# Kernel optimization log

Hardware: AMD Instinct MI355X
Metric: run time of the kernel (lower is better)

The kernel has to match this reference:

```python
import jax, jax.numpy as jnp
import numpy as np


def _fft_conv(x, filts):
    # x: [B, inC, S, S] real; filts: [inC, outC, k, k, 2] (real/imag channels)
    # Matches FFT_Conv_Layer: zero-pad bottom/right by k-1, FFT, complex
    # multiply-accumulate over inC, inverse FFT, crop [1:-1, 1:-1], take real.
    N = x.shape[-1] + filts.shape[-2] - 1  # imgSize + filtSize - 1
    Fx = jnp.fft.fft2(x, s=(N, N))                      # [B, inC, N, N] complex
    fc = filts[..., 0] + 1j * filts[..., 1]             # [inC, outC, k, k] complex
    Ff = jnp.fft.fft2(fc, s=(N, N))                     # [inC, outC, N, N]
    prod = jnp.einsum('bihw,iohw->bohw', Fx, Ff)        # sum over inC, no huge 5D temp
    return jnp.real(jnp.fft.ifft2(prod))[:, :, 1:-1, 1:-1]


def _spectral_pool(x, fsize):
    # Keep lowest `fsize` frequencies (corner crop of the FFT), inverse FFT, ReLU.
    F = jnp.fft.fft2(x)
    n = (fsize - 1) // 2
    tl = F[:, :, :n + 1, :n + 1]
    tr = F[:, :, :n + 1, -n:]
    bl = F[:, :, -n:, :n + 1]
    br = F[:, :, -n:, -n:]
    top = jnp.concatenate([tl, tr], axis=-1)
    bot = jnp.concatenate([bl, br], axis=-1)
    out = jnp.real(jnp.fft.ifft2(jnp.concatenate([top, bot], axis=-2)))
    return jax.nn.relu(out)


def setup_inputs() -> dict:
    key = jax.random.key(0)
    ks = jax.random.split(key, 10)
    B = 16
    filt_shapes = [(3, 32), (32, 64), (64, 128), (128, 256), (256, 256)]
    inp = {'x': jax.random.normal(ks[0], (B, 3, 224, 224), dtype=jnp.float32)}
    for i, (ci, co) in enumerate(filt_shapes):
        inp[f'f{i + 1}'] = 0.01 * jax.random.normal(ks[1 + i], (ci, co, 3, 3, 2), dtype=jnp.float32)
    inp['gamma'] = jnp.ones((256,), jnp.float32)
    inp['beta'] = jnp.zeros((256,), jnp.float32)
    inp['W1'] = 0.02 * jax.random.normal(ks[6], (9216, 512), dtype=jnp.float32)
    inp['b1'] = jnp.zeros((512,), jnp.float32)
    inp['W2'] = 0.02 * jax.random.normal(ks[7], (512, 256), dtype=jnp.float32)
    inp['b2'] = jnp.zeros((256,), jnp.float32)
    inp['W3'] = 0.02 * jax.random.normal(ks[8], (256, 10), dtype=jnp.float32)
    inp['b3'] = jnp.zeros((10,), jnp.float32)
    return inp


def reference(x, f1, f2, f3, f4, f5, gamma, beta, W1, b1, W2, b2, W3, b3):
    h = _spectral_pool(_fft_conv(x, f1), 113)   # [B, 32, 113, 113]
    h = _spectral_pool(_fft_conv(h, f2), 55)    # [B, 64, 55, 55]
    h = _spectral_pool(_fft_conv(h, f3), 27)    # [B, 128, 27, 27]
    h = _spectral_pool(_fft_conv(h, f4), 13)    # [B, 256, 13, 13]
    h = _fft_conv(h, f5)                        # [B, 256, 13, 13]
    # BatchNorm2d (training mode: batch statistics, biased variance)
    mean = jnp.mean(h, axis=(0, 2, 3), keepdims=True)
    var = jnp.var(h, axis=(0, 2, 3), keepdims=True)
    h = (h - mean) * jax.lax.rsqrt(var + 1e-5)
    h = h * gamma.reshape(1, -1, 1, 1) + beta.reshape(1, -1, 1, 1)
    # AdaptiveAvgPool2d((6,6)) on 13x13 == avg pool, kernel 3, stride 2
    h = jax.lax.reduce_window(h, 0.0, jax.lax.add, (1, 1, 3, 3), (1, 1, 2, 2), 'VALID') / 9.0
    h = h.reshape(h.shape[0], -1)               # [B, 9216]
    # dropout omitted (deterministic reference)
    h = jax.nn.relu(h @ W1 + b1)
    h = jax.nn.relu(h @ W2 + b2)
    return jax.nn.log_softmax(h @ W3 + b3, axis=1)
```

## Files before the change

kernel.cpp:

```cpp
#include <hip/hip_runtime.h>
#include <hip/hip_bf16.h>

typedef __attribute__((ext_vector_type(8))) short short8_t;
typedef __attribute__((ext_vector_type(4))) float float4_t;

#define OFF_CF  0u
#define OFF_PB1 25690112u
#define OFF_PB2 38765568u
#define OFF_PB3 44960768u
#define OFF_PB4 47946752u
#define OFF_C5  49331200u
#define OFF_AP  52100096u
#define OFF_H1  52689920u
#define OFF_H2  52722688u
#define OFF_P   52739072u
#define OFF_FPK 53918720u
#define OFF_PPK 55874560u

static __device__ __forceinline__ unsigned short f2bf(float v) {
    __hip_bfloat16 h = __float2bfloat16(v);
    return *(unsigned short*)&h;
}
static __device__ __forceinline__ float bf2f(unsigned short u) {
    __hip_bfloat16 h = *(__hip_bfloat16*)&u;
    return __bfloat162float(h);
}
static __device__ __forceinline__ unsigned short ld_bf(const float* p) { return f2bf(*p); }
static __device__ __forceinline__ unsigned short ld_bf(const unsigned short* p) { return *p; }
static __device__ __forceinline__ void st_out(float* p, float v) { *p = v; }
static __device__ __forceinline__ void st_out(unsigned short* p, float v) { *p = f2bf(v); }

__global__ void pack_f_k(const float* __restrict__ f, unsigned short* __restrict__ A,
                         int Ci, int Co) {
    int id = blockIdx.x * 256 + threadIdx.x;
    int nci = Ci >> 5;
    int total = (Co >> 4) * nci * 9 * 512;
    if (id >= total) return;
    int j = id & 7, lane = (id >> 3) & 63;
    int uv = (id >> 9) % 9;
    int rest = id / (512 * 9);
    int cc = rest % nci, co_blk = rest / nci;
    int m = lane & 15, k = ((lane >> 4) << 3) + j;
    int ci = (cc << 5) + k, co = (co_blk << 4) + m;
    A[id] = f2bf(f[((size_t)(ci * Co + co) * 9 + uv) * 2]);
}

__global__ void pack_f1_k(const float* __restrict__ f, unsigned short* __restrict__ A) {
    int id = blockIdx.x * 256 + threadIdx.x;
    if (id >= 2 * 512) return;
    int j = id & 7, lane = (id >> 3) & 63, co_blk = id >> 9;
    int m = lane & 15, k = ((lane >> 4) << 3) + j;
    float v = 0.f;
    if (k < 27) {
        int ci = k / 9, uv = k % 9;
        v = f[((size_t)(ci * 32 + co_blk * 16 + m) * 9 + uv) * 2];
    }
    A[id] = f2bf(v);
}

__global__ void pack_pool_k(unsigned short* __restrict__ P, int M, int N, int RT, int KC) {
    int id = blockIdx.x * 256 + threadIdx.x;
    if (id >= RT * KC * 512) return;
    int j = id & 7, lane = (id >> 3) & 63;
    int c = (id >> 9) % KC, rt = id / (512 * KC);
    int row = (rt << 4) + (lane & 15);
    int col = (c << 5) + ((lane >> 4) << 3) + j;
    double val = 0.0;
    if (row < M && col < N) {
        int n = (M - 1) / 2;
        double w = 6.283185307179586476925286766559 *
                   ((double)row / (double)M - (double)col / (double)N);
        double acc = 1.0;
        for (int a = 1; a <= n; ++a) acc += 2.0 * cos(w * (double)a);
        val = acc / (double)M;
    }
    float vf = (float)val;
    unsigned short hi = f2bf(vf);
    unsigned short lo = f2bf(vf - bf2f(hi));
    size_t base = ((size_t)(rt * KC + c) * 2) * 512 + lane * 8 + j;
    P[base] = hi;
    P[base + 512] = lo;
}

#define CPAD 40
template<typename Tin, typename Tout>
__global__ void conv_mfma_k(const Tin* __restrict__ x, const unsigned short* __restrict__ Apk,
                            Tout* __restrict__ y, int Ci, int Co, int H) {
    __shared__ unsigned short xs[3 * 34 * CPAD];
    int p = blockIdx.z % H, b = blockIdx.z / H;
    int q0 = blockIdx.x << 5;
    int co0 = blockIdx.y << 5;
    int tid = threadIdx.x;
    int lane = tid & 63, w = tid >> 6;
    int co_sub = w >> 1, n_sub = w & 1;
    int n_off = n_sub << 4;
    int nci = Ci >> 5;
    int kb = ((lane >> 4) << 3);
    float4_t acc = {0.f, 0.f, 0.f, 0.f};
    const Tin* xb = x + (size_t)b * Ci * H * H;
    int co_blk = (co0 >> 4) + co_sub;
    for (int cc = 0; cc < nci; ++cc) {
        for (int e = tid; e < 32 * 3 * 34; e += 256) {
            int ci = e / 102, rc = e % 102, r = rc / 34, c = rc % 34;
            int gp = p - 1 + r, gq = q0 - 1 + c;
            unsigned short v = 0;
            if ((unsigned)gp < (unsigned)H && (unsigned)gq < (unsigned)H)
                v = ld_bf(&xb[((size_t)((cc << 5) + ci) * H + gp) * H + gq]);
            xs[(r * 34 + c) * CPAD + ci] = v;
        }
        __syncthreads();
        const unsigned short* Ap = Apk + (((size_t)co_blk * nci + cc) * 9) * 512;
#pragma unroll
        for (int uv = 0; uv < 9; ++uv) {
            int u = uv / 3, v = uv % 3;
            short8_t af = *(const short8_t*)(Ap + ((uv * 64 + lane) << 3));
            int r = 2 - u;
            int c = n_off + (lane & 15) + 2 - v;
            short8_t bf = *(const short8_t*)(&xs[(r * 34 + c) * CPAD + kb]);
            acc = __builtin_amdgcn_mfma_f32_16x16x32_bf16(af, bf, acc, 0, 0, 0);
        }
        __syncthreads();
    }
    int n = lane & 15, mg = (lane >> 4) << 2;
    int q = q0 + n_off + n;
    if (q < H) {
        Tout* yb = y + (((size_t)b * Co + co0 + (co_sub << 4)) * H + p) * H + q;
#pragma unroll
        for (int r2 = 0; r2 < 4; ++r2)
            st_out(&yb[(size_t)(mg + r2) * H * H], acc[r2]);
    }
}

template<typename Tout>
__global__ void conv1_mfma_k(const float* __restrict__ x, const unsigned short* __restrict__ Apk,
                             Tout* __restrict__ y, int H) {
    __shared__ unsigned short xs[32 * CPAD];
    int p = blockIdx.z % H, b = blockIdx.z / H;
    int q0 = blockIdx.x << 5;
    int tid = threadIdx.x;
    int lane = tid & 63, w = tid >> 6;
    int co_sub = w >> 1, n_sub = w & 1;
    int n_off = n_sub << 4;
    int kb = ((lane >> 4) << 3);
    const float* xb = x + (size_t)b * 3 * H * H;
    for (int e = tid; e < 1024; e += 256) {
        int n = e >> 5, k = e & 31;
        float val = 0.f;
        if (k < 27) {
            int ci = k / 9, uv = k % 9, u = uv / 3, v = uv % 3;
            int gp = p + 1 - u, gq = q0 + n + 1 - v;
            if ((unsigned)gp < (unsigned)H && (unsigned)gq < (unsigned)H)
                val = xb[((size_t)ci * H + gp) * H + gq];
        }
        xs[n * CPAD + k] = f2bf(val);
    }
    __syncthreads();
    short8_t af = *(const short8_t*)(Apk + ((co_sub * 64 + lane) << 3));
    short8_t bf = *(const short8_t*)(&xs[(n_off + (lane & 15)) * CPAD + kb]);
    float4_t acc = {0.f, 0.f, 0.f, 0.f};
    acc = __builtin_amdgcn_mfma_f32_16x16x32_bf16(af, bf, acc, 0, 0, 0);
    int n = lane & 15, mg = (lane >> 4) << 2;
    int q = q0 + n_off + n;
    if (q < H) {
        Tout* yb = y + (((size_t)b * 32 + (co_sub << 4)) * H + p) * H + q;
#pragma unroll
        for (int r2 = 0; r2 < 4; ++r2)
            st_out(&yb[(size_t)(mg + r2) * H * H], acc[r2]);
    }
}

template<int N, int M, int TRT>
__global__ __launch_bounds__(256) void pool_mfma_k(const float* __restrict__ x,
                                                   const unsigned short* __restrict__ PK,
                                                   unsigned short* __restrict__ out) {
    constexpr int MT = (N + 15) / 16;
    constexpr int RT = (M + 15) / 16;
    constexpr int KC = (N + 31) / 32;
    constexpr int XPAD = 40;
    constexpr int ZPAD = KC * 32 + 8;
    constexpr int XROWS = MT * 16;
    constexpr int NT1 = MT * TRT;
    constexpr int L1 = (NT1 + 3) / 4;
    constexpr int NT2 = RT * TRT;
    constexpr int L2 = (NT2 + 3) / 4;
    __shared__ unsigned short xh[XROWS * XPAD], xl[XROWS * XPAD];
    __shared__ unsigned short zh[16 * TRT * ZPAD], zl[16 * TRT * ZPAD];

    int t0g = blockIdx.x * TRT;
    int bc = blockIdx.y;
    int tid = threadIdx.x;
    int lane = tid & 63, w = tid >> 6;
    int l15 = lane & 15;
    int kb = (lane >> 4) << 3;
    const float* xb = x + (size_t)bc * N * N;

    float4_t acc[L1];
#pragma unroll
    for (int i = 0; i < L1; ++i) acc[i] = (float4_t){0.f, 0.f, 0.f, 0.f};

    for (int c = 0; c < KC; ++c) {
        for (int id = tid; id < XROWS * 32; id += 256) {
            int u = id >> 5, vv = id & 31, v = (c << 5) + vv;
            float val = (u < N && v < N) ? xb[u * N + v] : 0.f;
            unsigned short hi = f2bf(val);
            xh[u * XPAD + vv] = hi;
            xl[u * XPAD + vv] = f2bf(val - bf2f(hi));
        }
        __syncthreads();
#pragma unroll
        for (int li = 0; li < L1; ++li) {
            int idx = li * 4 + w;
            if (idx < NT1) {
                int mt = idx / TRT, nt = idx % TRT;
                short8_t ahi = *(const short8_t*)(&xh[(mt * 16 + l15) * XPAD + kb]);
                short8_t alo = *(const short8_t*)(&xl[(mt * 16 + l15) * XPAD + kb]);
                const unsigned short* bp =
                    PK + ((size_t)((t0g + nt) * KC + c) * 2) * 512 + lane * 8;
                short8_t bhi = *(const short8_t*)bp;
                short8_t blo = *(const short8_t*)(bp + 512);
                acc[li] = __builtin_amdgcn_mfma_f32_16x16x32_bf16(ahi, bhi, acc[li], 0, 0, 0);
                acc[li] = __builtin_amdgcn_mfma_f32_16x16x32_bf16(ahi, blo, acc[li], 0, 0, 0);
                acc[li] = __builtin_amdgcn_mfma_f32_16x16x32_bf16(alo, bhi, acc[li], 0, 0, 0);
            }
        }
        __syncthreads();
    }
#pragma unroll
    for (int li = 0; li < L1; ++li) {
        int idx = li * 4 + w;
        if (idx < NT1) {
            int mt = idx / TRT, nt = idx % TRT;
            int t = nt * 16 + l15;
            int u0 = mt * 16 + ((lane >> 4) << 2);
            unsigned short h0 = f2bf(acc[li][0]), h1 = f2bf(acc[li][1]);
            unsigned short h2 = f2bf(acc[li][2]), h3 = f2bf(acc[li][3]);
            unsigned long long ph =
                (unsigned long long)h0 | ((unsigned long long)h1 << 16) |
                ((unsigned long long)h2 << 32) | ((unsigned long long)h3 << 48);
            unsigned long long pl =
                (unsigned long long)f2bf(acc[li][0] - bf2f(h0)) |
                ((unsigned long long)f2bf(acc[li][1] - bf2f(h1)) << 16) |
                ((unsigned long long)f2bf(acc[li][2] - bf2f(h2)) << 32) |
                ((unsigned long long)f2bf(acc[li][3] - bf2f(h3)) << 48);
            *(unsigned long long*)(&zh[t * ZPAD + u0]) = ph;
            *(unsigned long long*)(&zl[t * ZPAD + u0]) = pl;
        }
    }
    __syncthreads();

    float4_t acc2[L2];
#pragma unroll
    for (int i = 0; i < L2; ++i) acc2[i] = (float4_t){0.f, 0.f, 0.f, 0.f};
    for (int c = 0; c < KC; ++c) {
#pragma unroll
        for (int li = 0; li < L2; ++li) {
            int idx = li * 4 + w;
            if (idx < NT2) {
                int mt = idx / TRT, nt = idx % TRT;
                const unsigned short* ap =
                    PK + ((size_t)(mt * KC + c) * 2) * 512 + lane * 8;
                short8_t ahi = *(const short8_t*)ap;
                short8_t alo = *(const short8_t*)(ap + 512);
                short8_t bzh = *(const short8_t*)(&zh[(nt * 16 + l15) * ZPAD + (c << 5) + kb]);
                short8_t bzl = *(const short8_t*)(&zl[(nt * 16 + l15) * ZPAD + (c << 5) + kb]);
                acc2[li] = __builtin_amdgcn_mfma_f32_16x16x32_bf16(ahi, bzh, acc2[li], 0, 0, 0);
                acc2[li] = __builtin_amdgcn_mfma_f32_16x16x32_bf16(ahi, bzl, acc2[li], 0, 0, 0);
                acc2[li] = __builtin_amdgcn_mfma_f32_16x16x32_bf16(alo, bzh, acc2[li], 0, 0, 0);
            }
        }
    }
    unsigned short* ob = out + (size_t)bc * M * M;
#pragma unroll
    for (int li = 0; li < L2; ++li) {
        int idx = li * 4 + w;
        if (idx < NT2) {
            int mt = idx / TRT, nt = idx % TRT;
            int t = (t0g + nt) * 16 + l15;
            if (t < M) {
                int s0 = mt * 16 + ((lane >> 4) << 2);
#pragma unroll
                for (int r = 0; r < 4; ++r) {
                    int s = s0 + r;
                    if (s < M) ob[s * M + t] = f2bf(fmaxf(acc2[li][r], 0.f));
                }
            }
        }
    }
}

__global__ void bn_k(float* __restrict__ h, const float* __restrict__ gamma,
                     const float* __restrict__ beta) {
    int c = blockIdx.x;
    int tid = threadIdx.x;
    float s = 0.f, s2 = 0.f;
    for (int i = tid; i < 16 * 169; i += 256) {
        int b = i / 169, hw = i % 169;
        float v = h[((size_t)b * 256 + c) * 169 + hw];
        s += v; s2 += v * v;
    }
    __shared__ float red[256], red2[256];
    red[tid] = s; red2[tid] = s2;
    __syncthreads();
    for (int st = 128; st > 0; st >>= 1) {
        if (tid < st) { red[tid] += red[tid + st]; red2[tid] += red2[tid + st]; }
        __syncthreads();
    }
    __shared__ float sc, sh;
    if (tid == 0) {
        float mean = red[0] / (16.f * 169.f);
        float var  = red2[0] / (16.f * 169.f) - mean * mean;
        float inv  = rsqrtf(var + 1e-5f);
        sc = gamma[c] * inv;
        sh = beta[c] - mean * sc;
    }
    __syncthreads();
    for (int i = tid; i < 16 * 169; i += 256) {
        int b = i / 169, hw = i % 169;
        size_t idx = ((size_t)b * 256 + c) * 169 + hw;
        h[idx] = h[idx] * sc + sh;
    }
}

__global__ void avgpool_k(const float* __restrict__ h, float* __restrict__ ap) {
    int id = blockIdx.x * 256 + threadIdx.x;
    if (id >= 16 * 256 * 36) return;
    int j = id % 6, i = (id / 6) % 6, c = (id / 36) % 256, b = id / (36 * 256);
    const float* hb = h + ((size_t)b * 256 + c) * 169;
    float s = 0.f;
#pragma unroll
    for (int di = 0; di < 3; ++di)
#pragma unroll
        for (int dj = 0; dj < 3; ++dj)
            s += hb[(2 * i + di) * 13 + (2 * j + dj)];
    ap[(size_t)b * 9216 + c * 36 + i * 6 + j] = s * (1.f / 9.f);
}

template<int BATCH, int KLEN>
__global__ void fc_part_k(const float* __restrict__ h, const float* __restrict__ W,
                          float* __restrict__ P, int Kdim, int N) {
    __shared__ float hs[BATCH * KLEN];
    __shared__ float red[BATCH * 64];
    int tx = threadIdx.x, ty = threadIdx.y;
    int tid = ty * 64 + tx;
    int o = blockIdx.x * 64 + tx;
    int k0 = blockIdx.y * KLEN;
    for (int i = tid; i < BATCH * KLEN; i += 256) {
        int b = i / KLEN, k = i % KLEN;
        hs[i] = h[(size_t)b * Kdim + k0 + k];
    }
    __syncthreads();
    float acc[BATCH];
#pragma unroll
    for (int b = 0; b < BATCH; ++b) acc[b] = 0.f;
    for (int k = ty; k < KLEN; k += 4) {
        float w = W[(size_t)(k0 + k) * N + o];
#pragma unroll
        for (int b = 0; b < BATCH; ++b) acc[b] += hs[b * KLEN + k] * w;
    }
    for (int kz = 0; kz < 4; ++kz) {
        if (ty == kz) {
#pragma unroll
            for (int b = 0; b < BATCH; ++b) {
                if (kz == 0) red[b * 64 + tx] = acc[b];
                else         red[b * 64 + tx] += acc[b];
            }
        }
        __syncthreads();
    }
    if (ty == 0) {
#pragma unroll
        for (int b = 0; b < BATCH; ++b)
            P[((size_t)blockIdx.y * BATCH + b) * N + o] = red[b * 64 + tx];
    }
}

template<int BATCH>
__global__ void fc_reduce_k(const float* __restrict__ P, const float* __restrict__ bias,
                            float* __restrict__ out, int N, int KS, int relu) {
    int id = blockIdx.x * 256 + threadIdx.x;
    if (id >= BATCH * N) return;
    int b = id / N, o = id % N;
    float s = bias[o];
    for (int ks = 0; ks < KS; ++ks) s += P[((size_t)ks * BATCH + b) * N + o];
    if (relu) s = fmaxf(s, 0.f);
    out[(size_t)b * N + o] = s;
}

__global__ void fc3_softmax_k(const float* __restrict__ h, const float* __restrict__ W,
                              const float* __restrict__ bias, float* __restrict__ out) {
    int b = blockIdx.x;
    int o = threadIdx.x;
    __shared__ float l[10];
    if (o < 10) {
        float acc = bias[o];
        for (int k = 0; k < 256; ++k) acc += h[b * 256 + k] * W[k * 10 + o];
        l[o] = acc;
    }
    __syncthreads();
    if (o == 0) {
        float m = l[0];
        for (int i = 1; i < 10; ++i) m = fmaxf(m, l[i]);
        float s = 0.f;
        for (int i = 0; i < 10; ++i) s += expf(l[i] - m);
        float lse = m + logf(s);
        for (int i = 0; i < 10; ++i) out[b * 10 + i] = l[i] - lse;
    }
}

extern "C" void kernel_launch(void* const* d_in, const int* in_sizes, int n_in,
                              void* d_out, int out_size, void* d_ws, size_t ws_size,
                              hipStream_t stream) {
    const float* x     = (const float*)d_in[0];
    const float* f1    = (const float*)d_in[1];
    const float* f2    = (const float*)d_in[2];
    const float* f3    = (const float*)d_in[3];
    const float* f4    = (const float*)d_in[4];
    const float* f5    = (const float*)d_in[5];
    const float* gamma = (const float*)d_in[6];
    const float* beta  = (const float*)d_in[7];
    const float* W1    = (const float*)d_in[8];
    const float* b1    = (const float*)d_in[9];
    const float* W2    = (const float*)d_in[10];
    const float* b2    = (const float*)d_in[11];
    const float* W3    = (const float*)d_in[12];
    const float* b3    = (const float*)d_in[13];
    float* out = (float*)d_out;
    char* ws = (char*)d_ws;

    float* CF = (float*)(ws + OFF_CF);
    unsigned short* PB1 = (unsigned short*)(ws + OFF_PB1);
    unsigned short* PB2 = (unsigned short*)(ws + OFF_PB2);
    unsigned short* PB3 = (unsigned short*)(ws + OFF_PB3);
    unsigned short* PB4 = (unsigned short*)(ws + OFF_PB4);
    float* C5 = (float*)(ws + OFF_C5);
    float* AP = (float*)(ws + OFF_AP);
    float* H1 = (float*)(ws + OFF_H1);
    float* H2 = (float*)(ws + OFF_H2);
    float* P  = (float*)(ws + OFF_P);
    unsigned short* PK1 = (unsigned short*)(ws + OFF_FPK);
    unsigned short* PK2 = PK1 + 1024;
    unsigned short* PK3 = PK2 + 18432;
    unsigned short* PK4 = PK3 + 73728;
    unsigned short* PK5 = PK4 + 294912;
    unsigned short* PP1 = (unsigned short*)(ws + OFF_PPK);
    unsigned short* PP2 = PP1 + 57344;
    unsigned short* PP3 = PP2 + 16384;
    unsigned short* PP4 = PP3 + 4096;

    pack_f1_k<<<(2 * 512 + 255) / 256, 256, 0, stream>>>(f1, PK1);
    pack_f_k<<<(4 * 1 * 9 * 512 + 255) / 256, 256, 0, stream>>>(f2, PK2, 32, 64);
    pack_f_k<<<(8 * 2 * 9 * 512 + 255) / 256, 256, 0, stream>>>(f3, PK3, 64, 128);
    pack_f_k<<<(16 * 4 * 9 * 512 + 255) / 256, 256, 0, stream>>>(f4, PK4, 128, 256);
    pack_f_k<<<(16 * 8 * 9 * 512 + 255) / 256, 256, 0, stream>>>(f5, PK5, 256, 256);
    pack_pool_k<<<(8 * 7 * 512 + 255) / 256, 256, 0, stream>>>(PP1, 113, 224, 8, 7);
    pack_pool_k<<<(4 * 4 * 512 + 255) / 256, 256, 0, stream>>>(PP2, 55, 113, 4, 4);
    pack_pool_k<<<(2 * 2 * 512 + 255) / 256, 256, 0, stream>>>(PP3, 27, 55, 2, 2);
    pack_pool_k<<<(1 * 1 * 512 + 255) / 256, 256, 0, stream>>>(PP4, 13, 27, 1, 1);

    for (int ck = 0; ck < 4; ++ck) {
        int b0 = ck * 4;
        conv1_mfma_k<float><<<dim3(7, 1, 4 * 224), 256, 0, stream>>>(
            x + (size_t)b0 * 3 * 224 * 224, PK1, CF, 224);
        pool_mfma_k<224, 113, 4><<<dim3(2, 4 * 32), 256, 0, stream>>>(
            CF, PP1, PB1 + (size_t)b0 * 32 * 113 * 113);
    }
    for (int ck = 0; ck < 4; ++ck) {
        int b0 = ck * 4;
        conv_mfma_k<unsigned short, float><<<dim3(4, 2, 4 * 113), 256, 0, stream>>>(
            PB1 + (size_t)b0 * 32 * 113 * 113, PK2, CF, 32, 64, 113);
        pool_mfma_k<113, 55, 4><<<dim3(1, 4 * 64), 256, 0, stream>>>(
            CF, PP2, PB2 + (size_t)b0 * 64 * 55 * 55);
    }
    conv_mfma_k<unsigned short, float><<<dim3(2, 4, 16 * 55), 256, 0, stream>>>(
        PB2, PK3, CF, 64, 128, 55);
    pool_mfma_k<55, 27, 2><<<dim3(1, 16 * 128), 256, 0, stream>>>(CF, PP3, PB3);
    conv_mfma_k<unsigned short, float><<<dim3(1, 8, 16 * 27), 256, 0, stream>>>(
        PB3, PK4, CF, 128, 256, 27);
    pool_mfma_k<27, 13, 1><<<dim3(1, 16 * 256), 256, 0, stream>>>(CF, PP4, PB4);
    conv_mfma_k<unsigned short, float><<<dim3(1, 8, 16 * 13), 256, 0, stream>>>(
        PB4, PK5, C5, 256, 256, 13);

    bn_k<<<256, 256, 0, stream>>>(C5, gamma, beta);
    avgpool_k<<<(16 * 256 * 36 + 255) / 256, 256, 0, stream>>>(C5, AP);
    fc_part_k<16, 256><<<dim3(512 / 64, 36), dim3(64, 4), 0, stream>>>(AP, W1, P, 9216, 512);
    fc_reduce_k<16><<<(16 * 512 + 255) / 256, 256, 0, stream>>>(P, b1, H1, 512, 36, 1);
    fc_part_k<16, 64><<<dim3(256 / 64, 8), dim3(64, 4), 0, stream>>>(H1, W2, P, 512, 256);
    fc_reduce_k<16><<<(16 * 256 + 255) / 256, 256, 0, stream>>>(P, b2, H2, 256, 8, 1);
    fc3_softmax_k<<<16, 64, 0, stream>>>(H2, W3, b3, out);
}
```

Measured before the change: 781.0 us.

## Register-block conv MFMA kernel over output rows and channels with swizzled LDS

Replaces the per-row conv kernels with a templated conv_mfma2_k. Each block covers several output rows (PBLK) and a larger output-channel group, so loaded filter fragments and the staged input halo are reused across multiple accumulators, and LDS uses an XOR swizzle to avoid bank conflicts. Conv1 now goes through the generic path, with its input channels zero-padded to 32 instead of packing all 27 taps into K. This cuts the redundant halo reloads and per-row launch overhead at the cost of more registers and wasted MFMA work in the first layer.

```diff
diff --git a/kernel.cpp b/kernel.cpp
--- a/kernel.cpp
+++ b/kernel.cpp
@@ -15,7 +15,7 @@
 #define OFF_H2  52722688u
 #define OFF_P   52739072u
 #define OFF_FPK 53918720u
-#define OFF_PPK 55874560u
+#define OFF_PPK 55890944u
 
 static __device__ __forceinline__ unsigned short f2bf(float v) {
     __hip_bfloat16 h = __float2bfloat16(v);
@@ -31,7 +31,7 @@
 static __device__ __forceinline__ void st_out(unsigned short* p, float v) { *p = f2bf(v); }
 
 __global__ void pack_f_k(const float* __restrict__ f, unsigned short* __restrict__ A,
-                         int Ci, int Co) {
+                         int Ci, int Co, int CIR) {
     int id = blockIdx.x * 256 + threadIdx.x;
     int nci = Ci >> 5;
     int total = (Co >> 4) * nci * 9 * 512;
@@ -42,19 +42,7 @@
     int cc = rest % nci, co_blk = rest / nci;
     int m = lane & 15, k = ((lane >> 4) << 3) + j;
     int ci = (cc << 5) + k, co = (co_blk << 4) + m;
-    A[id] = f2bf(f[((size_t)(ci * Co + co) * 9 + uv) * 2]);
-}
-
-__global__ void pack_f1_k(const float* __restrict__ f, unsigned short* __restrict__ A) {
-    int id = blockIdx.x * 256 + threadIdx.x;
-    if (id >= 2 * 512) return;
-    int j = id & 7, lane = (id >> 3) & 63, co_blk = id >> 9;
-    int m = lane & 15, k = ((lane >> 4) << 3) + j;
-    float v = 0.f;
-    if (k < 27) {
-        int ci = k / 9, uv = k % 9;
-        v = f[((size_t)(ci * 32 + co_blk * 16 + m) * 9 + uv) * 2];
-    }
+    float v = (ci < CIR) ? f[((size_t)(ci * Co + co) * 9 + uv) * 2] : 0.f;
     A[id] = f2bf(v);
 }
 
@@ -82,90 +70,85 @@
     P[base + 512] = lo;
 }
 
-#define CPAD 40
-template<typename Tin, typename Tout>
-__global__ void conv_mfma_k(const Tin* __restrict__ x, const unsigned short* __restrict__ Apk,
-                            Tout* __restrict__ y, int Ci, int Co, int H) {
-    __shared__ unsigned short xs[3 * 34 * CPAD];
-    int p = blockIdx.z % H, b = blockIdx.z / H;
-    int q0 = blockIdx.x << 5;
-    int co0 = blockIdx.y << 5;
+template<int CI, int CIR, int CO, int COB, int PBLK, int WQT, typename Tin, typename Tout>
+__global__ __launch_bounds__(256) void conv_mfma2_k(const Tin* __restrict__ x,
+        const unsigned short* __restrict__ Apk, Tout* __restrict__ y, int H) {
+    constexpr int ROWS = PBLK + 2;
+    constexpr int QW = WQT * 16 + 2;
+    constexpr int RC = ROWS * QW;
+    constexpr int NCC = CI >> 5;
+    constexpr int NCOG = CO / COB;
+    constexpr int NC = (WQT == 2) ? (COB / 32) : (COB / 64);
+    __shared__ unsigned short xs[RC * 40];
+    int b = blockIdx.z / NCOG;
+    int co0 = (blockIdx.z % NCOG) * COB;
+    int q0 = blockIdx.x * (WQT * 16);
+    int p0 = blockIdx.y * PBLK;
     int tid = threadIdx.x;
     int lane = tid & 63, w = tid >> 6;
-    int co_sub = w >> 1, n_sub = w & 1;
-    int n_off = n_sub << 4;
-    int nci = Ci >> 5;
-    int kb = ((lane >> 4) << 3);
-    float4_t acc = {0.f, 0.f, 0.f, 0.f};
-    const Tin* xb = x + (size_t)b * Ci * H * H;
-    int co_blk = (co0 >> 4) + co_sub;
-    for (int cc = 0; cc < nci; ++cc) {
-        for (int e = tid; e < 32 * 3 * 34; e += 256) {
-            int ci = e / 102, rc = e % 102, r = rc / 34, c = rc % 34;
-            int gp = p - 1 + r, gq = q0 - 1 + c;
+    int l15 = lane & 15;
+    int kch = lane >> 4;
+    int mg = kch << 2;
+    int qt = (WQT == 2) ? (w & 1) : 0;
+    int ctb = (WQT == 2) ? ((w >> 1) * NC) : (w * NC);
+    const Tin* xb = x + (size_t)b * CIR * H * H;
+    float4_t acc[PBLK][NC];
+#pragma unroll
+    for (int pr = 0; pr < PBLK; ++pr)
+#pragma unroll
+        for (int nc = 0; nc < NC; ++nc) acc[pr][nc] = (float4_t){0.f, 0.f, 0.f, 0.f};
+    for (int cc = 0; cc < NCC; ++cc) {
+        for (int i = tid; i < RC * 32; i += 256) {
+            int ci = i / RC;
+            int rc = i - ci * RC;
+            int r = rc / QW;
+            int c = rc - r * QW;
+            int gp = p0 - 1 + r, gq = q0 - 1 + c;
             unsigned short v = 0;
-            if ((unsigned)gp < (unsigned)H && (unsigned)gq < (unsigned)H)
+            if ((CI == CIR || ((cc << 5) + ci) < CIR) &&
+                (unsigned)gp < (unsigned)H && (unsigned)gq < (unsigned)H)
                 v = ld_bf(&xb[((size_t)((cc << 5) + ci) * H + gp) * H + gq]);
-            xs[(r * 34 + c) * CPAD + ci] = v;
-        }
-        __syncthreads();
-        const unsigned short* Ap = Apk + (((size_t)co_blk * nci + cc) * 9) * 512;
+            xs[rc * 40 + ((((ci >> 3) ^ ((rc >> 3) & 3)) << 3) | (ci & 7))] = v;
+        }
+        __syncthreads();
 #pragma unroll
         for (int uv = 0; uv < 9; ++uv) {
-            int u = uv / 3, v = uv % 3;
-            short8_t af = *(const short8_t*)(Ap + ((uv * 64 + lane) << 3));
-            int r = 2 - u;
-            int c = n_off + (lane & 15) + 2 - v;
-            short8_t bf = *(const short8_t*)(&xs[(r * 34 + c) * CPAD + kb]);
-            acc = __builtin_amdgcn_mfma_f32_16x16x32_bf16(af, bf, acc, 0, 0, 0);
-        }
-        __syncthreads();
-    }
-    int n = lane & 15, mg = (lane >> 4) << 2;
-    int q = q0 + n_off + n;
+            const int u = uv / 3, v = uv % 3;
+            short8_t af[NC];
+#pragma unroll
+            for (int nc = 0; nc < NC; ++nc) {
+                int ct = (co0 >> 4) + ctb + nc;
+                af[nc] = *(const short8_t*)(Apk +
+                    (((size_t)ct * NCC + cc) * 9 + uv) * 512 + lane * 8);
+            }
+#pragma unroll
+            for (int pr = 0; pr < PBLK; ++pr) {
+                int rcL = (pr + 2 - u) * QW + qt * 16 + (2 - v) + l15;
+                int addr = rcL * 40 + ((kch ^ ((rcL >> 3) & 3)) << 3);
+                short8_t bf = *(const short8_t*)(&xs[addr]);
+#pragma unroll
+                for (int nc = 0; nc < NC; ++nc)
+                    acc[pr][nc] = __builtin_amdgcn_mfma_f32_16x16x32_bf16(
+                        af[nc], bf, acc[pr][nc], 0, 0, 0);
+            }
+        }
+        __syncthreads();
+    }
+    int q = q0 + qt * 16 + l15;
     if (q < H) {
-        Tout* yb = y + (((size_t)b * Co + co0 + (co_sub << 4)) * H + p) * H + q;
-#pragma unroll
-        for (int r2 = 0; r2 < 4; ++r2)
-            st_out(&yb[(size_t)(mg + r2) * H * H], acc[r2]);
-    }
-}
-
-template<typename Tout>
-__global__ void conv1_mfma_k(const float* __restrict__ x, const unsigned short* __restrict__ Apk,
-                             Tout* __restrict__ y, int H) {
-    __shared__ unsigned short xs[32 * CPAD];
-    int p = blockIdx.z % H, b = blockIdx.z / H;
-    int q0 = blockIdx.x << 5;
-    int tid = threadIdx.x;
-    int lane = tid & 63, w = tid >> 6;
-    int co_sub = w >> 1, n_sub = w & 1;
-    int n_off = n_sub << 4;
-    int kb = ((lane >> 4) << 3);
-    const float* xb = x + (size_t)b * 3 * H * H;
-    for (int e = tid; e < 1024; e += 256) {
-        int n = e >> 5, k = e & 31;
-        float val = 0.f;
-        if (k < 27) {
-            int ci = k / 9, uv = k % 9, u = uv / 3, v = uv % 3;
-            int gp = p + 1 - u, gq = q0 + n + 1 - v;
-            if ((unsigned)gp < (unsigned)H && (unsigned)gq < (unsigned)H)
-                val = xb[((size_t)ci * H + gp) * H + gq];
-        }
-        xs[n * CPAD + k] = f2bf(val);
-    }
-    __syncthreads();
-    short8_t af = *(const short8_t*)(Apk + ((co_sub * 64 + lane) << 3));
-    short8_t bf = *(const short8_t*)(&xs[(n_off + (lane & 15)) * CPAD + kb]);
-    float4_t acc = {0.f, 0.f, 0.f, 0.f};
-    acc = __builtin_amdgcn_mfma_f32_16x16x32_bf16(af, bf, acc, 0, 0, 0);
-    int n = lane & 15, mg = (lane >> 4) << 2;
-    int q = q0 + n_off + n;
-    if (q < H) {
-        Tout* yb = y + (((size_t)b * 32 + (co_sub << 4)) * H + p) * H + q;
-#pragma unroll
-        for (int r2 = 0; r2 < 4; ++r2)
-            st_out(&yb[(size_t)(mg + r2) * H * H], acc[r2]);
+#pragma unroll
+        for (int pr = 0; pr < PBLK; ++pr) {
+            int p = p0 + pr;
+            if (p < H) {
+#pragma unroll
+                for (int nc = 0; nc < NC; ++nc) {
+                    Tout* yb = y + (((size_t)b * CO + co0 + (ctb + nc) * 16 + mg) * H + p) * H + q;
+#pragma unroll
+                    for (int r2 = 0; r2 < 4; ++r2)
+                        st_out(&yb[(size_t)r2 * H * H], acc[pr][nc][r2]);
+                }
+            }
+        }
     }
 }
 
@@ -438,7 +421,7 @@
     float* H2 = (float*)(ws + OFF_H2);
     float* P  = (float*)(ws + OFF_P);
     unsigned short* PK1 = (unsigned short*)(ws + OFF_FPK);
-    unsigned short* PK2 = PK1 + 1024;
+    unsigned short* PK2 = PK1 + 9216;
     unsigned short* PK3 = PK2 + 18432;
     unsigned short* PK4 = PK3 + 73728;
     unsigned short* PK5 = PK4 + 294912;
@@ -447,11 +430,11 @@
     unsigned short* PP3 = PP2 + 16384;
     unsigned short* PP4 = PP3 + 4096;
 
-    pack_f1_k<<<(2 * 512 + 255) / 256, 256, 0, stream>>>(f1, PK1);
-    pack_f_k<<<(4 * 1 * 9 * 512 + 255) / 256, 256, 0, stream>>>(f2, PK2, 32, 64);
-    pack_f_k<<<(8 * 2 * 9 * 512 + 255) / 256, 256, 0, stream>>>(f3, PK3, 64, 128);
-    pack_f_k<<<(16 * 4 * 9 * 512 + 255) / 256, 256, 0, stream>>>(f4, PK4, 128, 256);
-    pack_f_k<<<(16 * 8 * 9 * 512 + 255) / 256, 256, 0, stream>>>(f5, PK5, 256, 256);
+    pack_f_k<<<36,   256, 0, stream>>>(f1, PK1, 32, 32, 3);
+    pack_f_k<<<72,   256, 0, stream>>>(f2, PK2, 32, 64, 32);
+    pack_f_k<<<288,  256, 0, stream>>>(f3, PK3, 64, 128, 64);
+    pack_f_k<<<1152, 256, 0, stream>>>(f4, PK4, 128, 256, 128);
+    pack_f_k<<<2304, 256, 0, stream>>>(f5, PK5, 256, 256, 256);
     pack_pool_k<<<(8 * 7 * 512 + 255) / 256, 256, 0, stream>>>(PP1, 113, 224, 8, 7);
     pack_pool_k<<<(4 * 4 * 512 + 255) / 256, 256, 0, stream>>>(PP2, 55, 113, 4, 4);
     pack_pool_k<<<(2 * 2 * 512 + 255) / 256, 256, 0, stream>>>(PP3, 27, 55, 2, 2);
@@ -459,26 +442,26 @@
 
     for (int ck = 0; ck < 4; ++ck) {
         int b0 = ck * 4;
-        conv1_mfma_k<float><<<dim3(7, 1, 4 * 224), 256, 0, stream>>>(
-            x + (size_t)b0 * 3 * 224 * 224, PK1, CF, 224);
+        conv_mfma2_k<32, 3, 32, 32, 6, 2, float, float>
+            <<<dim3(7, 38, 4), 256, 0, stream>>>(x + (size_t)b0 * 3 * 224 * 224, PK1, CF, 224);
         pool_mfma_k<224, 113, 4><<<dim3(2, 4 * 32), 256, 0, stream>>>(
             CF, PP1, PB1 + (size_t)b0 * 32 * 113 * 113);
     }
     for (int ck = 0; ck < 4; ++ck) {
         int b0 = ck * 4;
-        conv_mfma_k<unsigned short, float><<<dim3(4, 2, 4 * 113), 256, 0, stream>>>(
-            PB1 + (size_t)b0 * 32 * 113 * 113, PK2, CF, 32, 64, 113);
+        conv_mfma2_k<32, 32, 64, 64, 6, 2, unsigned short, float>
+            <<<dim3(4, 19, 4), 256, 0, stream>>>(PB1 + (size_t)b0 * 32 * 113 * 113, PK2, CF, 113);
         pool_mfma_k<113, 55, 4><<<dim3(1, 4 * 64), 256, 0, stream>>>(
             CF, PP2, PB2 + (size_t)b0 * 64 * 55 * 55);
     }
-    conv_mfma_k<unsigned short, float><<<dim3(2, 4, 16 * 55), 256, 0, stream>>>(
-        PB2, PK3, CF, 64, 128, 55);
+    conv_mfma2_k<64, 64, 128, 128, 6, 2, unsigned short, float>
+        <<<dim3(2, 10, 16), 256, 0, stream>>>(PB2, PK3, CF, 55);
     pool_mfma_k<55, 27, 2><<<dim3(1, 16 * 128), 256, 0, stream>>>(CF, PP3, PB3);
-    conv_mfma_k<unsigned short, float><<<dim3(1, 8, 16 * 27), 256, 0, stream>>>(
-        PB3, PK4, CF, 128, 256, 27);
+    conv_mfma2_k<128, 128, 256, 128, 4, 2, unsigned short, float>
+        <<<dim3(1, 7, 32), 256, 0, stream>>>(PB3, PK4, CF, 27);
     pool_mfma_k<27, 13, 1><<<dim3(1, 16 * 256), 256, 0, stream>>>(CF, PP4, PB4);
-    conv_mfma_k<unsigned short, float><<<dim3(1, 8, 16 * 13), 256, 0, stream>>>(
-        PB4, PK5, C5, 256, 256, 13);
+    conv_mfma2_k<256, 256, 256, 128, 2, 1, unsigned short, float>
+        <<<dim3(1, 7, 32), 256, 0, stream>>>(PB4, PK5, C5, 13);
 
     bn_k<<<256, 256, 0, stream>>>(C5, gamma, beta);
     avgpool_k<<<(16 * 256 * 36 + 255) / 256, 256, 0, stream>>>(C5, AP);
```

After: 777.7 us. About the same (-0.4%).
